# Optimization experiments

Measured on AMD Instinct MI355X. Metric: run time of the kernel, lower is better.

## Reference

```python
import jax, jax.numpy as jnp
import numpy as np

B, T, J, E = 64, 512, 64, 128
D = 2 * E  # bidaf feature dim


def _lstm_dir(x, Wih, Whh, bih, bhh, reverse):
    # x: (B, S, I); PyTorch gate order i, f, g, o
    H = Whh.shape[1]
    b = bih + bhh
    xs = jnp.swapaxes(x, 0, 1)  # (S, B, I)
    if reverse:
        xs = xs[::-1]
    pre = jnp.einsum('sbi,gi->sbg', xs, Wih) + b  # precompute input projections
    h0 = jnp.zeros((x.shape[0], H), x.dtype)

    def step(carry, pt):
        h, c = carry
        gates = pt + h @ Whh.T
        i, f, g, o = jnp.split(gates, 4, axis=-1)
        c = jax.nn.sigmoid(f) * c + jax.nn.sigmoid(i) * jnp.tanh(g)
        h = jax.nn.sigmoid(o) * jnp.tanh(c)
        return (h, c), h

    _, hs = jax.lax.scan(step, (h0, h0), pre)
    if reverse:
        hs = hs[::-1]
    return jnp.swapaxes(hs, 0, 1)  # (B, S, H)


def _bilstm(x, pf, pb):
    hf = _lstm_dir(x, pf[0], pf[1], pf[2], pf[3], False)
    hb = _lstm_dir(x, pb[0], pb[1], pb[2], pb[3], True)
    return jnp.concatenate([hf, hb], axis=-1)


def setup_inputs() -> dict:
    key = jax.random.key(0)
    ks = iter(jax.random.split(key, 40))

    def rn(shape, scale=0.05):
        return jax.random.normal(next(ks), shape, jnp.float32) * scale

    inp = {
        'c': jax.random.normal(next(ks), (B, T, D), jnp.float32),
        'q': jax.random.normal(next(ks), (B, J, D), jnp.float32),
        # trilinear attention weights (Linear(2E,1) each)
        'wc': rn((D,)), 'bc': rn((1,)),
        'wq': rn((D,)), 'bq': rn((1,)),
        'wcq': rn((D,)), 'bcq': rn((1,)),
        # modeling BiLSTM: input 8E -> hidden E, bidirectional
        'l1f_Wih': rn((4 * E, 8 * E)), 'l1f_Whh': rn((4 * E, E)), 'l1f_bih': rn((4 * E,)), 'l1f_bhh': rn((4 * E,)),
        'l1b_Wih': rn((4 * E, 8 * E)), 'l1b_Whh': rn((4 * E, E)), 'l1b_bih': rn((4 * E,)), 'l1b_bhh': rn((4 * E,)),
        # output BiLSTM: input 2E -> hidden E, bidirectional
        'l2f_Wih': rn((4 * E, 2 * E)), 'l2f_Whh': rn((4 * E, E)), 'l2f_bih': rn((4 * E,)), 'l2f_bhh': rn((4 * E,)),
        'l2b_Wih': rn((4 * E, 2 * E)), 'l2b_Whh': rn((4 * E, E)), 'l2b_bih': rn((4 * E,)), 'l2b_bhh': rn((4 * E,)),
        # span predictors Linear(10E, 1)
        'W0': rn((10 * E,)), 'b0': rn((1,)),
        'W1': rn((10 * E,)), 'b1': rn((1,)),
    }
    return inp


def reference(c, q, wc, bc, wq, bq, wcq, bcq,
              l1f_Wih, l1f_Whh, l1f_bih, l1f_bhh,
              l1b_Wih, l1b_Whh, l1b_bih, l1b_bhh,
              l2f_Wih, l2f_Whh, l2f_bih, l2f_bhh,
              l2b_Wih, l2b_Whh, l2b_bih, l2b_bhh,
              W0, b0, W1, b1):
    # fused trilinear similarity: replaces the python loop over q_len
    cq = jnp.einsum('btd,bjd,d->btj', c, q, wcq) + bcq[0]            # (B,T,J)
    s = (c @ wc + bc[0])[:, :, None] + (q @ wq + bq[0])[:, None, :] + cq
    a = jax.nn.softmax(s, axis=2)
    c2q = jnp.einsum('btj,bjd->btd', a, q)                            # context-to-query
    b_att = jax.nn.softmax(jnp.max(s, axis=2), axis=1)                # (B,T)
    q2c = jnp.einsum('bt,btd->bd', b_att, c)[:, None, :]              # (B,1,2E) broadcast over T
    g = jnp.concatenate([c, c2q, c * c2q, c * q2c * jnp.ones_like(c)], axis=-1)  # (B,T,8E)

    m = _bilstm(g, (l1f_Wih, l1f_Whh, l1f_bih, l1f_bhh), (l1b_Wih, l1b_Whh, l1b_bih, l1b_bhh))
    p1 = jax.nn.softmax(jnp.concatenate([g, m], axis=-1) @ W0 + b0[0], axis=1)
    m2 = _bilstm(m, (l2f_Wih, l2f_Whh, l2f_bih, l2f_bhh), (l2b_Wih, l2b_Whh, l2b_bih, l2b_bhh))
    p2 = jax.nn.softmax(jnp.concatenate([g, m2], axis=-1) @ W1 + b1[0], axis=1)
    return (p1, p2)
```

## Files before the change

kernel.cpp:

```cpp
#include <hip/hip_runtime.h>
#include <hip/hip_bf16.h>
#include <cstdint>
#include <cstddef>


typedef short short8v __attribute__((ext_vector_type(8)));
typedef float f32x4 __attribute__((ext_vector_type(4)));
typedef unsigned short ushort8v __attribute__((ext_vector_type(8)));
typedef unsigned short ushort4v __attribute__((ext_vector_type(4)));

static __device__ __forceinline__ float bf2f(unsigned short u) {
  return __uint_as_float(((unsigned int)u) << 16);
}
static __device__ __forceinline__ unsigned short f2bf(float f) {
  unsigned int u = __float_as_uint(f);
  return (unsigned short)((u + 0x7FFFu + ((u >> 16) & 1u)) >> 16);
}
static __device__ __forceinline__ float fsig(float x) {
  return 1.f / (1.f + __expf(-x));
}
static __device__ __forceinline__ float ftanh(float x) {
  return 1.f - 2.f / (__expf(2.f * x) + 1.f);
}

__global__ __launch_bounds__(256) void cvt_w_kernel(
    const float* __restrict__ w1f, const float* __restrict__ w1b,
    const float* __restrict__ w2f, const float* __restrict__ w2b,
    const float* __restrict__ b1fi, const float* __restrict__ b1fh,
    const float* __restrict__ b1bi, const float* __restrict__ b1bh,
    const float* __restrict__ b2fi, const float* __restrict__ b2fh,
    const float* __restrict__ b2bi, const float* __restrict__ b2bh,
    unsigned short* __restrict__ d1f, unsigned short* __restrict__ d1b,
    unsigned short* __restrict__ d2f, unsigned short* __restrict__ d2b,
    float* __restrict__ bs)
{
  const int bid = blockIdx.x, tid = threadIdx.x;
  if (bid < 1280) {
    int idx = (bid * 256 + tid) * 4;
    const float* src;
    unsigned short* dst;
    int off;
    if (idx < 524288)        { src = w1f; dst = d1f; off = idx; }
    else if (idx < 1048576)  { src = w1b; dst = d1b; off = idx - 524288; }
    else if (idx < 1179648)  { src = w2f; dst = d2f; off = idx - 1048576; }
    else                     { src = w2b; dst = d2b; off = idx - 1179648; }
    float4 f = *(const float4*)(src + off);
    ushort4v v;
    v[0] = f2bf(f.x); v[1] = f2bf(f.y); v[2] = f2bf(f.z); v[3] = f2bf(f.w);
    *(ushort4v*)(dst + off) = v;
  } else {
    int bidx = (bid - 1280) * 256 + tid;
    int which = bidx >> 9, col = bidx & 511;
    float v;
    if (which == 0)      v = b1fi[col] + b1fh[col];
    else if (which == 1) v = b1bi[col] + b1bh[col];
    else if (which == 2) v = b2fi[col] + b2fh[col];
    else                 v = b2bi[col] + b2bh[col];
    bs[bidx] = v;
  }
}

__global__ __launch_bounds__(256) void attn_kernel(
    const float* __restrict__ c, const float* __restrict__ q,
    const float* __restrict__ wc, const float* __restrict__ bc,
    const float* __restrict__ wq, const float* __restrict__ bq,
    const float* __restrict__ wcq, const float* __restrict__ bcq,
    const float* __restrict__ W0, const float* __restrict__ W1,
    __hip_bfloat16* __restrict__ g, float* __restrict__ smax,
    float* __restrict__ gz0, float* __restrict__ gz1)
{
  __shared__ unsigned short cbf[128][264];
  __shared__ unsigned short qhb[64][264];
  __shared__ unsigned short qtb[256][72];
  __shared__ unsigned short Pbuf[4][16][72];
  __shared__ float qwqs[64];
  __shared__ float qwp[4][64];
  const int b = blockIdx.x, tid = threadIdx.x;
  const int wave = tid >> 6, lane = tid & 63;
  const int t0 = blockIdx.y * 128;
  unsigned short* gbase = (unsigned short*)g;

  #pragma unroll
  for (int i = 0; i < 16; ++i) {
    int idx = tid + i * 256;
    int j = idx >> 6, d4 = (idx & 63) * 4;
    float4 v = *(const float4*)&q[((size_t)b * 64 + j) * 256 + d4];
    float4 w4 = *(const float4*)&wcq[d4];
    float4 c4 = *(const float4*)&wc[d4];
    qhb[j][d4 + 0] = f2bf(v.x * w4.x + c4.x);
    qhb[j][d4 + 1] = f2bf(v.y * w4.y + c4.y);
    qhb[j][d4 + 2] = f2bf(v.z * w4.z + c4.z);
    qhb[j][d4 + 3] = f2bf(v.w * w4.w + c4.w);
    qtb[d4 + 0][j] = f2bf(v.x);
    qtb[d4 + 1][j] = f2bf(v.y);
    qtb[d4 + 2][j] = f2bf(v.z);
    qtb[d4 + 3][j] = f2bf(v.w);
  }
  #pragma unroll
  for (int i = 0; i < 32; ++i) {
    int idx = tid + i * 256;
    int r = idx >> 6, d4 = (idx & 63) * 4;
    float4 v = *(const float4*)&c[((size_t)b * 512 + t0 + r) * 256 + d4];
    ushort4v u;
    u[0] = f2bf(v.x); u[1] = f2bf(v.y); u[2] = f2bf(v.z); u[3] = f2bf(v.w);
    *(ushort4v*)&cbf[r][d4] = u;
    *(ushort4v*)&gbase[((size_t)b * 512 + t0 + r) * 1024 + d4] = u;
  }
  __syncthreads();
  {
    float s = 0.f;
    for (int dd = 0; dd < 64; ++dd) {
      int d = wave * 64 + dd;
      s += bf2f(qtb[d][lane]) * wq[d];
    }
    qwp[wave][lane] = s;
  }
  __syncthreads();
  if (tid < 64) qwqs[tid] = qwp[0][tid] + qwp[1][tid] + qwp[2][tid] + qwp[3][tid] + bq[0];
  __syncthreads();

  const int cl = lane & 15, kg = lane >> 4;
  const float sbias = bc[0] + bcq[0];

  #pragma unroll
  for (int half = 0; half < 2; ++half) {
    const int tt = wave + half * 4;
    const int rowb = tt * 16;
    f32x4 acc[4] = {};
    #pragma unroll
    for (int kt = 0; kt < 8; ++kt) {
      short8v a = *(const short8v*)&cbf[rowb + cl][kt * 32 + kg * 8];
      #pragma unroll
      for (int jt = 0; jt < 4; ++jt) {
        short8v bq_ = *(const short8v*)&qhb[jt * 16 + cl][kt * 32 + kg * 8];
        acc[jt] = __builtin_amdgcn_mfma_f32_16x16x32_bf16(a, bq_, acc[jt], 0, 0, 0);
      }
    }
    #pragma unroll
    for (int jt = 0; jt < 4; ++jt) {
      float qadd = qwqs[jt * 16 + cl] + sbias;
      #pragma unroll
      for (int r = 0; r < 4; ++r) acc[jt][r] += qadd;
    }
    f32x4 mx = acc[0];
    #pragma unroll
    for (int jt = 1; jt < 4; ++jt)
      #pragma unroll
      for (int r = 0; r < 4; ++r) mx[r] = fmaxf(mx[r], acc[jt][r]);
    #pragma unroll
    for (int off = 1; off < 16; off <<= 1)
      #pragma unroll
      for (int r = 0; r < 4; ++r) mx[r] = fmaxf(mx[r], __shfl_xor(mx[r], off));
    f32x4 se = {0.f, 0.f, 0.f, 0.f};
    #pragma unroll
    for (int jt = 0; jt < 4; ++jt)
      #pragma unroll
      for (int r = 0; r < 4; ++r) {
        acc[jt][r] = __expf(acc[jt][r] - mx[r]);
        se[r] += acc[jt][r];
      }
    #pragma unroll
    for (int off = 1; off < 16; off <<= 1)
      #pragma unroll
      for (int r = 0; r < 4; ++r) se[r] += __shfl_xor(se[r], off);
    f32x4 inv;
    #pragma unroll
    for (int r = 0; r < 4; ++r) inv[r] = 1.f / se[r];
    #pragma unroll
    for (int jt = 0; jt < 4; ++jt)
      #pragma unroll
      for (int r = 0; r < 4; ++r)
        Pbuf[wave][4 * kg + r][jt * 16 + cl] = f2bf(acc[jt][r] * inv[r]);
    if (cl == 0) {
      #pragma unroll
      for (int r = 0; r < 4; ++r)
        smax[(size_t)b * 512 + t0 + rowb + 4 * kg + r] = mx[r];
    }
    f32x4 gz0p = {0.f, 0.f, 0.f, 0.f}, gz1p = {0.f, 0.f, 0.f, 0.f};
    for (int dt = 0; dt < 16; ++dt) {
      f32x4 ca = {0.f, 0.f, 0.f, 0.f};
      #pragma unroll
      for (int kt = 0; kt < 2; ++kt) {
        short8v pa = *(const short8v*)&Pbuf[wave][cl][kt * 32 + kg * 8];
        short8v qb_ = *(const short8v*)&qtb[dt * 16 + cl][kt * 32 + kg * 8];
        ca = __builtin_amdgcn_mfma_f32_16x16x32_bf16(pa, qb_, ca, 0, 0, 0);
      }
      int d = dt * 16 + cl;
      float w0a = W0[d], w0b_ = W0[256 + d], w0c2 = W0[512 + d];
      float w1a = W1[d], w1b2 = W1[256 + d], w1c2 = W1[512 + d];
      #pragma unroll
      for (int r = 0; r < 4; ++r) {
        int rloc = rowb + 4 * kg + r;
        float cv = bf2f(cbf[rloc][d]);
        float av = ca[r];
        float pr = cv * av;
        size_t gr = ((size_t)b * 512 + t0 + rloc) * 1024;
        gbase[gr + 256 + d] = f2bf(av);
        gbase[gr + 512 + d] = f2bf(pr);
        gz0p[r] += cv * w0a + av * w0b_ + pr * w0c2;
        gz1p[r] += cv * w1a + av * w1b2 + pr * w1c2;
      }
    }
    #pragma unroll
    for (int off = 1; off < 16; off <<= 1)
      #pragma unroll
      for (int r = 0; r < 4; ++r) {
        gz0p[r] += __shfl_xor(gz0p[r], off);
        gz1p[r] += __shfl_xor(gz1p[r], off);
      }
    if (cl == 0) {
      #pragma unroll
      for (int r = 0; r < 4; ++r) {
        size_t rw = (size_t)b * 512 + t0 + rowb + 4 * kg + r;
        gz0[rw] = gz0p[r];
        gz1[rw] = gz1p[r];
      }
    }
  }
}

__global__ __launch_bounds__(256) void batt_kernel(
    const float* __restrict__ c, const float* __restrict__ smax,
    const float* __restrict__ W0, const float* __restrict__ W1,
    __hip_bfloat16* __restrict__ g,
    float* __restrict__ gz0, float* __restrict__ gz1)
{
  __shared__ float sm[512];
  __shared__ float red[4], red2[4];
  __shared__ float q2c_s[256];
  const int b = blockIdx.x, tid = threadIdx.x;
  float v0 = smax[(size_t)b * 512 + tid];
  float v1 = smax[(size_t)b * 512 + tid + 256];
  float m = fmaxf(v0, v1);
  #pragma unroll
  for (int off = 32; off; off >>= 1) m = fmaxf(m, __shfl_xor(m, off));
  if ((tid & 63) == 0) red[tid >> 6] = m;
  __syncthreads();
  float M = fmaxf(fmaxf(red[0], red[1]), fmaxf(red[2], red[3]));
  float e0 = expf(v0 - M), e1 = expf(v1 - M);
  float ssum = e0 + e1;
  #pragma unroll
  for (int off = 32; off; off >>= 1) ssum += __shfl_xor(ssum, off);
  if ((tid & 63) == 0) red2[tid >> 6] = ssum;
  __syncthreads();
  float S = red2[0] + red2[1] + red2[2] + red2[3];
  sm[tid] = e0 / S;
  sm[tid + 256] = e1 / S;
  __syncthreads();
  float acc = 0.f;
  #pragma unroll 8
  for (int t = 0; t < 512; ++t) acc += sm[t] * c[((size_t)b * 512 + t) * 256 + tid];
  q2c_s[tid] = acc;
  __syncthreads();
  const int wave = tid >> 6, lane = tid & 63;
  float qv[4], w0c[4], w1c[4];
  #pragma unroll
  for (int r = 0; r < 4; ++r) {
    int d = lane + 64 * r;
    qv[r]  = q2c_s[d];
    w0c[r] = W0[768 + d];
    w1c[r] = W1[768 + d];
  }
  for (int t = wave; t < 512; t += 4) {
    size_t row = (size_t)b * 512 + t;
    float s0 = 0.f, s1 = 0.f;
    #pragma unroll
    for (int r = 0; r < 4; ++r) {
      int d = lane + 64 * r;
      float v = c[row * 256 + d];
      float gv = v * qv[r];
      g[row * 1024 + 768 + d] = __float2bfloat16(gv);
      s0 += gv * w0c[r];
      s1 += gv * w1c[r];
    }
    #pragma unroll
    for (int off = 32; off; off >>= 1) {
      s0 += __shfl_xor(s0, off);
      s1 += __shfl_xor(s1, off);
    }
    if (lane == 0) { gz0[row] += s0; gz1[row] += s1; }
  }
}

__global__ __launch_bounds__(256) void gemm_mfma_kernel(
    const __hip_bfloat16* __restrict__ Xg,
    const unsigned short* __restrict__ Wf, const unsigned short* __restrict__ Wb,
    const float* __restrict__ bsf, const float* __restrict__ bsb,
    __hip_bfloat16* __restrict__ Yf, __hip_bfloat16* __restrict__ Yb, int K)
{
  __shared__ unsigned short Xs[128 * 72];
  __shared__ unsigned short Ws[128 * 72];
  const unsigned short* X = (const unsigned short*)Xg;
  const unsigned short* W = blockIdx.z ? Wb : Wf;
  const float* bs = blockIdx.z ? bsb : bsf;
  __hip_bfloat16* Y = blockIdx.z ? Yb : Yf;
  const int tid = threadIdx.x;
  const int m0 = blockIdx.x * 128, n0 = blockIdx.y * 128;
  const int lane = tid & 63, wave = tid >> 6;
  const int wr = wave >> 1, wc = wave & 1;
  const int frow = lane & 15, fk = (lane >> 4) * 8;

  f32x4 acc[4][4] = {};
  for (int kt = 0; kt < K; kt += 64) {
    #pragma unroll
    for (int i = 0; i < 4; ++i) {
      int cidx = tid + 256 * i;
      int row = cidx >> 3, kc = cidx & 7;
      *(ushort8v*)&Xs[row * 72 + kc * 8] =
          *(const ushort8v*)&X[(size_t)(m0 + row) * K + kt + kc * 8];
      *(ushort8v*)&Ws[row * 72 + kc * 8] =
          *(const ushort8v*)&W[(size_t)(n0 + row) * K + kt + kc * 8];
    }
    __syncthreads();
    #pragma unroll
    for (int kk = 0; kk < 64; kk += 32) {
      short8v a[4], bfr[4];
      #pragma unroll
      for (int i = 0; i < 4; ++i)
        a[i] = *(const short8v*)&Xs[(wr * 64 + i * 16 + frow) * 72 + kk + fk];
      #pragma unroll
      for (int j = 0; j < 4; ++j)
        bfr[j] = *(const short8v*)&Ws[(wc * 64 + j * 16 + frow) * 72 + kk + fk];
      #pragma unroll
      for (int i = 0; i < 4; ++i)
        #pragma unroll
        for (int j = 0; j < 4; ++j)
          acc[i][j] = __builtin_amdgcn_mfma_f32_16x16x32_bf16(a[i], bfr[j], acc[i][j], 0, 0, 0);
    }
    __syncthreads();
  }
  const int r0 = (lane >> 4) * 4;
  #pragma unroll
  for (int j = 0; j < 4; ++j) {
    int col = n0 + wc * 64 + j * 16 + (lane & 15);
    int colp = (col & 127) * 4 + (col >> 7);
    float bsum = bs[col];
    #pragma unroll
    for (int i = 0; i < 4; ++i) {
      int rowb = m0 + wr * 64 + i * 16 + r0;
      #pragma unroll
      for (int r = 0; r < 4; ++r)
        Y[(size_t)(rowb + r) * 512 + colp] = __float2bfloat16(acc[i][j][r] + bsum);
    }
  }
}

__global__ __launch_bounds__(512, 2) void lstm_kernel(
    const __hip_bfloat16* __restrict__ pre_f, const __hip_bfloat16* __restrict__ pre_b,
    const float* __restrict__ Whh_f, const float* __restrict__ Whh_b,
    __hip_bfloat16* __restrict__ out)
{
  const int b = blockIdx.x, dir = blockIdx.y;
  const unsigned short* __restrict__ pre =
      (const unsigned short*)(dir ? pre_b : pre_f);
  const float* __restrict__ Whh = dir ? Whh_b : Whh_f;
  const int off = dir ? 128 : 0;
  const int tid = threadIdx.x;
  const int wave = tid >> 6, lane = tid & 63;
  const int cl = lane & 15;
  const int kg = lane >> 4;
  const int cell = wave * 16 + cl;

#define LOAD_BF(Q, T, DST)                                            \
  {                                                                   \
    const float* wp = Whh + (size_t)(Q * 128 + cell) * 128 + T * 32 + kg * 8; \
    float4 f0 = *(const float4*)wp;                                   \
    float4 f1 = *(const float4*)(wp + 4);                             \
    DST[0] = (short)f2bf(f0.x); DST[1] = (short)f2bf(f0.y);           \
    DST[2] = (short)f2bf(f0.z); DST[3] = (short)f2bf(f0.w);           \
    DST[4] = (short)f2bf(f1.x); DST[5] = (short)f2bf(f1.y);           \
    DST[6] = (short)f2bf(f1.z); DST[7] = (short)f2bf(f1.w);           \
    asm volatile("" : "+v"(DST));                                     \
  }
  short8v bf00, bf01, bf02, bf03, bf10, bf11, bf12, bf13;
  short8v bf20, bf21, bf22, bf23, bf30, bf31, bf32, bf33;
  LOAD_BF(0, 0, bf00) LOAD_BF(0, 1, bf01) LOAD_BF(0, 2, bf02) LOAD_BF(0, 3, bf03)
  LOAD_BF(1, 0, bf10) LOAD_BF(1, 1, bf11) LOAD_BF(1, 2, bf12) LOAD_BF(1, 3, bf13)
  LOAD_BF(2, 0, bf20) LOAD_BF(2, 1, bf21) LOAD_BF(2, 2, bf22) LOAD_BF(2, 3, bf23)
  LOAD_BF(3, 0, bf30) LOAD_BF(3, 1, bf31) LOAD_BF(3, 2, bf32) LOAD_BF(3, 3, bf33)
#undef LOAD_BF

  __shared__ unsigned short hbuf[2][128];
  if (tid < 128) { hbuf[0][tid] = 0; hbuf[1][tid] = 0; }
  __syncthreads();

  const size_t base = (size_t)b * 512;
  const int tstep = dir ? -1 : 1;
  const int t0 = dir ? 511 : 0;
  const unsigned short* prow = pre + base * 512 + cell * 4;
  unsigned short* orow = (unsigned short*)out + base * 256 + off + cell;

  int cur = 0;
  float cst = 0.f;
  f32x4 acc0 = {0.f, 0.f, 0.f, 0.f};
  f32x4 acc1 = acc0, acc2 = acc0, acc3 = acc0;

#define LSTM_STEP(P, HOUT)                                                  \
  {                                                                         \
    const unsigned short* hb = hbuf[cur];                                   \
    short8v a0 = *(const short8v*)(hb +  0 + kg * 8);                       \
    short8v a1 = *(const short8v*)(hb + 32 + kg * 8);                       \
    short8v a2 = *(const short8v*)(hb + 64 + kg * 8);                       \
    short8v a3 = *(const short8v*)(hb + 96 + kg * 8);                       \
    acc0[0] = bf2f(P[0]); acc1[0] = bf2f(P[1]);                             \
    acc2[0] = bf2f(P[2]); acc3[0] = bf2f(P[3]);                             \
    acc0 = __builtin_amdgcn_mfma_f32_16x16x32_bf16(a0, bf00, acc0, 0, 0, 0);\
    acc1 = __builtin_amdgcn_mfma_f32_16x16x32_bf16(a0, bf10, acc1, 0, 0, 0);\
    acc2 = __builtin_amdgcn_mfma_f32_16x16x32_bf16(a0, bf20, acc2, 0, 0, 0);\
    acc3 = __builtin_amdgcn_mfma_f32_16x16x32_bf16(a0, bf30, acc3, 0, 0, 0);\
    acc0 = __builtin_amdgcn_mfma_f32_16x16x32_bf16(a1, bf01, acc0, 0, 0, 0);\
    acc1 = __builtin_amdgcn_mfma_f32_16x16x32_bf16(a1, bf11, acc1, 0, 0, 0);\
    acc2 = __builtin_amdgcn_mfma_f32_16x16x32_bf16(a1, bf21, acc2, 0, 0, 0);\
    acc3 = __builtin_amdgcn_mfma_f32_16x16x32_bf16(a1, bf31, acc3, 0, 0, 0);\
    acc0 = __builtin_amdgcn_mfma_f32_16x16x32_bf16(a2, bf02, acc0, 0, 0, 0);\
    acc1 = __builtin_amdgcn_mfma_f32_16x16x32_bf16(a2, bf12, acc1, 0, 0, 0);\
    acc2 = __builtin_amdgcn_mfma_f32_16x16x32_bf16(a2, bf22, acc2, 0, 0, 0);\
    acc3 = __builtin_amdgcn_mfma_f32_16x16x32_bf16(a2, bf32, acc3, 0, 0, 0);\
    acc0 = __builtin_amdgcn_mfma_f32_16x16x32_bf16(a3, bf03, acc0, 0, 0, 0);\
    acc1 = __builtin_amdgcn_mfma_f32_16x16x32_bf16(a3, bf13, acc1, 0, 0, 0);\
    acc2 = __builtin_amdgcn_mfma_f32_16x16x32_bf16(a3, bf23, acc2, 0, 0, 0);\
    acc3 = __builtin_amdgcn_mfma_f32_16x16x32_bf16(a3, bf33, acc3, 0, 0, 0);\
    float gi_ = fsig(acc0[0]);                                              \
    float gf_ = fsig(acc1[0]);                                              \
    float gg_ = ftanh(acc2[0]);                                             \
    float go_ = fsig(acc3[0]);                                              \
    cst = gf_ * cst + gi_ * gg_;                                            \
    float hv = go_ * ftanh(cst);                                            \
    HOUT = f2bf(hv);                                                        \
    if (lane < 16) hbuf[cur ^ 1][cell] = HOUT;                              \
    __syncthreads();                                                        \
    cur ^= 1;                                                               \
  }

  for (int chunk = 0; chunk < 64; ++chunk) {
    const int tb = t0 + chunk * 8 * tstep;
    ushort4v p0 = *(const ushort4v*)(prow + (size_t)(tb)             * 512);
    ushort4v p1 = *(const ushort4v*)(prow + (size_t)(tb + 1 * tstep) * 512);
    ushort4v p2 = *(const ushort4v*)(prow + (size_t)(tb + 2 * tstep) * 512);
    ushort4v p3 = *(const ushort4v*)(prow + (size_t)(tb + 3 * tstep) * 512);
    ushort4v p4 = *(const ushort4v*)(prow + (size_t)(tb + 4 * tstep) * 512);
    ushort4v p5 = *(const ushort4v*)(prow + (size_t)(tb + 5 * tstep) * 512);
    ushort4v p6 = *(const ushort4v*)(prow + (size_t)(tb + 6 * tstep) * 512);
    ushort4v p7 = *(const ushort4v*)(prow + (size_t)(tb + 7 * tstep) * 512);
    unsigned short h0, h1, h2, h3, h4, h5, h6, h7;
    LSTM_STEP(p0, h0)
    LSTM_STEP(p1, h1)
    LSTM_STEP(p2, h2)
    LSTM_STEP(p3, h3)
    LSTM_STEP(p4, h4)
    LSTM_STEP(p5, h5)
    LSTM_STEP(p6, h6)
    LSTM_STEP(p7, h7)
    if (lane < 16) {
      orow[(size_t)(tb)             * 256] = h0;
      orow[(size_t)(tb + 1 * tstep) * 256] = h1;
      orow[(size_t)(tb + 2 * tstep) * 256] = h2;
      orow[(size_t)(tb + 3 * tstep) * 256] = h3;
      orow[(size_t)(tb + 4 * tstep) * 256] = h4;
      orow[(size_t)(tb + 5 * tstep) * 256] = h5;
      orow[(size_t)(tb + 6 * tstep) * 256] = h6;
      orow[(size_t)(tb + 7 * tstep) * 256] = h7;
    }
  }
#undef LSTM_STEP
}

__global__ __launch_bounds__(256) void logits_kernel(
    const __hip_bfloat16* __restrict__ m, const float* __restrict__ W,
    const float* __restrict__ bias, const float* __restrict__ gz,
    float* __restrict__ z)
{
  const int row = blockIdx.x * 4 + (threadIdx.x >> 6);
  const int lane = threadIdx.x & 63;
  const unsigned short* mrow = (const unsigned short*)m + (size_t)row * 256;
  float acc = 0.f;
  #pragma unroll
  for (int i = 0; i < 4; ++i) acc += bf2f(mrow[lane + 64 * i]) * W[1024 + lane + 64 * i];
  #pragma unroll
  for (int off = 32; off; off >>= 1) acc += __shfl_xor(acc, off);
  if (lane == 0) z[row] = acc + gz[row] + bias[0];
}

__global__ __launch_bounds__(512) void softmax_t_kernel(
    const float* __restrict__ z, float* __restrict__ p)
{
  const int b = blockIdx.x, t = threadIdx.x;
  __shared__ float red[8], red2[8];
  float v = z[(size_t)b * 512 + t];
  float m = v;
  #pragma unroll
  for (int off = 32; off; off >>= 1) m = fmaxf(m, __shfl_xor(m, off));
  if ((t & 63) == 0) red[t >> 6] = m;
  __syncthreads();
  float M = red[0];
  #pragma unroll
  for (int i = 1; i < 8; ++i) M = fmaxf(M, red[i]);
  float e = expf(v - M);
  float s = e;
  #pragma unroll
  for (int off = 32; off; off >>= 1) s += __shfl_xor(s, off);
  if ((t & 63) == 0) red2[t >> 6] = s;
  __syncthreads();
  float S = red2[0];
  #pragma unroll
  for (int i = 1; i < 8; ++i) S += red2[i];
  p[(size_t)b * 512 + t] = e / S;
}

extern "C" void kernel_launch(void* const* d_in, const int* in_sizes, int n_in,
                              void* d_out, int out_size, void* d_ws, size_t ws_size,
                              hipStream_t stream)
{
  const float* c   = (const float*)d_in[0];
  const float* q   = (const float*)d_in[1];
  const float* wc  = (const float*)d_in[2];
  const float* bc  = (const float*)d_in[3];
  const float* wq  = (const float*)d_in[4];
  const float* bq  = (const float*)d_in[5];
  const float* wcq = (const float*)d_in[6];
  const float* bcq = (const float*)d_in[7];
  const float* l1f_Wih = (const float*)d_in[8];
  const float* l1f_Whh = (const float*)d_in[9];
  const float* l1f_bih = (const float*)d_in[10];
  const float* l1f_bhh = (const float*)d_in[11];
  const float* l1b_Wih = (const float*)d_in[12];
  const float* l1b_Whh = (const float*)d_in[13];
  const float* l1b_bih = (const float*)d_in[14];
  const float* l1b_bhh = (const float*)d_in[15];
  const float* l2f_Wih = (const float*)d_in[16];
  const float* l2f_Whh = (const float*)d_in[17];
  const float* l2f_bih = (const float*)d_in[18];
  const float* l2f_bhh = (const float*)d_in[19];
  const float* l2b_Wih = (const float*)d_in[20];
  const float* l2b_Whh = (const float*)d_in[21];
  const float* l2b_bih = (const float*)d_in[22];
  const float* l2b_bhh = (const float*)d_in[23];
  const float* W0 = (const float*)d_in[24];
  const float* b0 = (const float*)d_in[25];
  const float* W1 = (const float*)d_in[26];
  const float* b1 = (const float*)d_in[27];

  const size_t required = 137371648u;
  if (ws_size < required) return;

  char* wsb = (char*)d_ws;
  __hip_bfloat16* gbf = (__hip_bfloat16*)wsb;
  __hip_bfloat16* m   = (__hip_bfloat16*)wsb;
  __hip_bfloat16* m2  = (__hip_bfloat16*)(wsb + 33554432);
  __hip_bfloat16* pref = (__hip_bfloat16*)(wsb + 67108864);
  __hip_bfloat16* preb = (__hip_bfloat16*)(wsb + 100663296);
  float* gz0  = (float*)(wsb + 134217728);
  float* gz1  = gz0 + 32768;
  float* smax = gz1 + 32768;
  float* z    = smax + 32768;
  unsigned short* w1f = (unsigned short*)(wsb + 134742016);
  unsigned short* w1b = (unsigned short*)(wsb + 135790592);
  unsigned short* w2f = (unsigned short*)(wsb + 136839168);
  unsigned short* w2b = (unsigned short*)(wsb + 137101312);
  float* bs = (float*)(wsb + 137363456);
  float* p1 = (float*)d_out;
  float* p2 = p1 + 32768;

  cvt_w_kernel<<<1288, 256, 0, stream>>>(l1f_Wih, l1b_Wih, l2f_Wih, l2b_Wih,
                                         l1f_bih, l1f_bhh, l1b_bih, l1b_bhh,
                                         l2f_bih, l2f_bhh, l2b_bih, l2b_bhh,
                                         w1f, w1b, w2f, w2b, bs);
  attn_kernel<<<dim3(64, 4), 256, 0, stream>>>(c, q, wc, bc, wq, bq, wcq, bcq,
                                               W0, W1, gbf, smax, gz0, gz1);
  batt_kernel<<<64, 256, 0, stream>>>(c, smax, W0, W1, gbf, gz0, gz1);

  gemm_mfma_kernel<<<dim3(256, 4, 2), 256, 0, stream>>>(
      gbf, w1f, w1b, bs, bs + 512, pref, preb, 1024);
  lstm_kernel<<<dim3(64, 2), 512, 0, stream>>>(pref, preb, l1f_Whh, l1b_Whh, m);

  logits_kernel<<<8192, 256, 0, stream>>>(m, W0, b0, gz0, z);
  softmax_t_kernel<<<64, 512, 0, stream>>>(z, p1);

  gemm_mfma_kernel<<<dim3(256, 4, 2), 256, 0, stream>>>(
      m, w2f, w2b, bs + 1024, bs + 1536, pref, preb, 256);
  lstm_kernel<<<dim3(64, 2), 512, 0, stream>>>(pref, preb, l2f_Whh, l2b_Whh, m2);

  logits_kernel<<<8192, 256, 0, stream>>>(m2, W1, b1, gz1, z);
  softmax_t_kernel<<<64, 512, 0, stream>>>(z, p2);
}
```

Measured before the change: 967.1 us.

## Split LSTM recurrence across 16 waves with gate-interleaved MFMA columns

The LSTM kernel now runs 1024 threads (16 waves) per batch/direction block instead of 512. Each wave computes 32 gate columns laid out interleaved (i,f,g,o per cell), with 8 MFMAs per step instead of 16. Activations are gathered across lanes with shuffles to form the cell update. This halves the serial MFMA chain per step and the weight registers per thread, at the cost of a wider barrier across more waves, extra shuffles, and scalar 2-byte pre-activation loads in place of vector loads.

```diff
diff --git a/kernel.cpp b/kernel.cpp
--- a/kernel.cpp
+++ b/kernel.cpp
@@ -345,7 +345,7 @@
   }
 }
 
-__global__ __launch_bounds__(512, 2) void lstm_kernel(
+__global__ __launch_bounds__(1024) void lstm_kernel(
     const __hip_bfloat16* __restrict__ pre_f, const __hip_bfloat16* __restrict__ pre_b,
     const float* __restrict__ Whh_f, const float* __restrict__ Whh_b,
     __hip_bfloat16* __restrict__ out)
@@ -359,25 +359,28 @@
   const int wave = tid >> 6, lane = tid & 63;
   const int cl = lane & 15;
   const int kg = lane >> 4;
-  const int cell = wave * 16 + cl;
-
-#define LOAD_BF(Q, T, DST)                                            \
-  {                                                                   \
-    const float* wp = Whh + (size_t)(Q * 128 + cell) * 128 + T * 32 + kg * 8; \
-    float4 f0 = *(const float4*)wp;                                   \
-    float4 f1 = *(const float4*)(wp + 4);                             \
-    DST[0] = (short)f2bf(f0.x); DST[1] = (short)f2bf(f0.y);           \
-    DST[2] = (short)f2bf(f0.z); DST[3] = (short)f2bf(f0.w);           \
-    DST[4] = (short)f2bf(f1.x); DST[5] = (short)f2bf(f1.y);           \
-    DST[6] = (short)f2bf(f1.z); DST[7] = (short)f2bf(f1.w);           \
-    asm volatile("" : "+v"(DST));                                     \
-  }
-  short8v bf00, bf01, bf02, bf03, bf10, bf11, bf12, bf13;
-  short8v bf20, bf21, bf22, bf23, bf30, bf31, bf32, bf33;
-  LOAD_BF(0, 0, bf00) LOAD_BF(0, 1, bf01) LOAD_BF(0, 2, bf02) LOAD_BF(0, 3, bf03)
-  LOAD_BF(1, 0, bf10) LOAD_BF(1, 1, bf11) LOAD_BF(1, 2, bf12) LOAD_BF(1, 3, bf13)
-  LOAD_BF(2, 0, bf20) LOAD_BF(2, 1, bf21) LOAD_BF(2, 2, bf22) LOAD_BF(2, 3, bf23)
-  LOAD_BF(3, 0, bf30) LOAD_BF(3, 1, bf31) LOAD_BF(3, 2, bf32) LOAD_BF(3, 3, bf33)
+  const int q3 = cl & 3;
+  const int lbase = lane & ~3;
+  const int cellA = 8 * wave + (cl >> 2);
+  const int cellB = cellA + 4;
+  const int nA = 32 * wave + cl;
+  const int nB = nA + 16;
+
+#define LOAD_BF(N, KT, DST)                                                 \
+  {                                                                         \
+    const float* wp = Whh + (size_t)(((N) & 3) * 128 + ((N) >> 2)) * 128 +  \
+                      (KT) * 32 + kg * 8;                                   \
+    float4 f0 = *(const float4*)wp;                                         \
+    float4 f1 = *(const float4*)(wp + 4);                                   \
+    DST[0] = (short)f2bf(f0.x); DST[1] = (short)f2bf(f0.y);                 \
+    DST[2] = (short)f2bf(f0.z); DST[3] = (short)f2bf(f0.w);                 \
+    DST[4] = (short)f2bf(f1.x); DST[5] = (short)f2bf(f1.y);                 \
+    DST[6] = (short)f2bf(f1.z); DST[7] = (short)f2bf(f1.w);                 \
+    asm volatile("" : "+v"(DST));                                           \
+  }
+  short8v b00, b01, b02, b03, b10, b11, b12, b13;
+  LOAD_BF(nA, 0, b00) LOAD_BF(nA, 1, b01) LOAD_BF(nA, 2, b02) LOAD_BF(nA, 3, b03)
+  LOAD_BF(nB, 0, b10) LOAD_BF(nB, 1, b11) LOAD_BF(nB, 2, b12) LOAD_BF(nB, 3, b13)
 #undef LOAD_BF
 
   __shared__ unsigned short hbuf[2][128];
@@ -387,79 +390,98 @@
   const size_t base = (size_t)b * 512;
   const int tstep = dir ? -1 : 1;
   const int t0 = dir ? 511 : 0;
-  const unsigned short* prow = pre + base * 512 + cell * 4;
-  unsigned short* orow = (unsigned short*)out + base * 256 + off + cell;
+  const unsigned short* prowA = pre + base * 512 + nA;
+  const unsigned short* prowB = pre + base * 512 + nB;
+  unsigned short* orowA = (unsigned short*)out + base * 256 + off + cellA;
+  unsigned short* orowB = (unsigned short*)out + base * 256 + off + cellB;
+  const bool writer = (kg == 0) && (q3 == 0);
 
   int cur = 0;
-  float cst = 0.f;
+  float cstA = 0.f, cstB = 0.f;
   f32x4 acc0 = {0.f, 0.f, 0.f, 0.f};
-  f32x4 acc1 = acc0, acc2 = acc0, acc3 = acc0;
-
-#define LSTM_STEP(P, HOUT)                                                  \
+  f32x4 acc1 = acc0;
+
+#define LSTM_STEP(PA, PB, HA, HB)                                           \
   {                                                                         \
     const unsigned short* hb = hbuf[cur];                                   \
     short8v a0 = *(const short8v*)(hb +  0 + kg * 8);                       \
     short8v a1 = *(const short8v*)(hb + 32 + kg * 8);                       \
     short8v a2 = *(const short8v*)(hb + 64 + kg * 8);                       \
     short8v a3 = *(const short8v*)(hb + 96 + kg * 8);                       \
-    acc0[0] = bf2f(P[0]); acc1[0] = bf2f(P[1]);                             \
-    acc2[0] = bf2f(P[2]); acc3[0] = bf2f(P[3]);                             \
-    acc0 = __builtin_amdgcn_mfma_f32_16x16x32_bf16(a0, bf00, acc0, 0, 0, 0);\
-    acc1 = __builtin_amdgcn_mfma_f32_16x16x32_bf16(a0, bf10, acc1, 0, 0, 0);\
-    acc2 = __builtin_amdgcn_mfma_f32_16x16x32_bf16(a0, bf20, acc2, 0, 0, 0);\
-    acc3 = __builtin_amdgcn_mfma_f32_16x16x32_bf16(a0, bf30, acc3, 0, 0, 0);\
-    acc0 = __builtin_amdgcn_mfma_f32_16x16x32_bf16(a1, bf01, acc0, 0, 0, 0);\
-    acc1 = __builtin_amdgcn_mfma_f32_16x16x32_bf16(a1, bf11, acc1, 0, 0, 0);\
-    acc2 = __builtin_amdgcn_mfma_f32_16x16x32_bf16(a1, bf21, acc2, 0, 0, 0);\
-    acc3 = __builtin_amdgcn_mfma_f32_16x16x32_bf16(a1, bf31, acc3, 0, 0, 0);\
-    acc0 = __builtin_amdgcn_mfma_f32_16x16x32_bf16(a2, bf02, acc0, 0, 0, 0);\
-    acc1 = __builtin_amdgcn_mfma_f32_16x16x32_bf16(a2, bf12, acc1, 0, 0, 0);\
-    acc2 = __builtin_amdgcn_mfma_f32_16x16x32_bf16(a2, bf22, acc2, 0, 0, 0);\
-    acc3 = __builtin_amdgcn_mfma_f32_16x16x32_bf16(a2, bf32, acc3, 0, 0, 0);\
-    acc0 = __builtin_amdgcn_mfma_f32_16x16x32_bf16(a3, bf03, acc0, 0, 0, 0);\
-    acc1 = __builtin_amdgcn_mfma_f32_16x16x32_bf16(a3, bf13, acc1, 0, 0, 0);\
-    acc2 = __builtin_amdgcn_mfma_f32_16x16x32_bf16(a3, bf23, acc2, 0, 0, 0);\
-    acc3 = __builtin_amdgcn_mfma_f32_16x16x32_bf16(a3, bf33, acc3, 0, 0, 0);\
-    float gi_ = fsig(acc0[0]);                                              \
-    float gf_ = fsig(acc1[0]);                                              \
-    float gg_ = ftanh(acc2[0]);                                             \
-    float go_ = fsig(acc3[0]);                                              \
-    cst = gf_ * cst + gi_ * gg_;                                            \
-    float hv = go_ * ftanh(cst);                                            \
-    HOUT = f2bf(hv);                                                        \
-    if (lane < 16) hbuf[cur ^ 1][cell] = HOUT;                              \
+    acc0[0] = bf2f(PA); acc1[0] = bf2f(PB);                                 \
+    acc0 = __builtin_amdgcn_mfma_f32_16x16x32_bf16(a0, b00, acc0, 0, 0, 0); \
+    acc1 = __builtin_amdgcn_mfma_f32_16x16x32_bf16(a0, b10, acc1, 0, 0, 0); \
+    acc0 = __builtin_amdgcn_mfma_f32_16x16x32_bf16(a1, b01, acc0, 0, 0, 0); \
+    acc1 = __builtin_amdgcn_mfma_f32_16x16x32_bf16(a1, b11, acc1, 0, 0, 0); \
+    acc0 = __builtin_amdgcn_mfma_f32_16x16x32_bf16(a2, b02, acc0, 0, 0, 0); \
+    acc1 = __builtin_amdgcn_mfma_f32_16x16x32_bf16(a2, b12, acc1, 0, 0, 0); \
+    acc0 = __builtin_amdgcn_mfma_f32_16x16x32_bf16(a3, b03, acc0, 0, 0, 0); \
+    acc1 = __builtin_amdgcn_mfma_f32_16x16x32_bf16(a3, b13, acc1, 0, 0, 0); \
+    float x0 = acc0[0], x1 = acc1[0];                                       \
+    float av0 = (q3 == 2) ? ftanh(x0) : fsig(x0);                           \
+    float av1 = (q3 == 2) ? ftanh(x1) : fsig(x1);                           \
+    float gi0 = __shfl(av0, lbase),     gf0 = __shfl(av0, lbase + 1);       \
+    float gg0 = __shfl(av0, lbase + 2), go0 = __shfl(av0, lbase + 3);       \
+    float gi1 = __shfl(av1, lbase),     gf1 = __shfl(av1, lbase + 1);       \
+    float gg1 = __shfl(av1, lbase + 2), go1 = __shfl(av1, lbase + 3);       \
+    cstA = gf0 * cstA + gi0 * gg0;                                          \
+    cstB = gf1 * cstB + gi1 * gg1;                                          \
+    float hv0 = go0 * ftanh(cstA);                                          \
+    float hv1 = go1 * ftanh(cstB);                                          \
+    HA = f2bf(hv0); HB = f2bf(hv1);                                         \
+    if (writer) {                                                           \
+      hbuf[cur ^ 1][cellA] = HA;                                            \
+      hbuf[cur ^ 1][cellB] = HB;                                            \
+    }                                                                       \
     __syncthreads();                                                        \
     cur ^= 1;                                                               \
   }
 
   for (int chunk = 0; chunk < 64; ++chunk) {
     const int tb = t0 + chunk * 8 * tstep;
-    ushort4v p0 = *(const ushort4v*)(prow + (size_t)(tb)             * 512);
-    ushort4v p1 = *(const ushort4v*)(prow + (size_t)(tb + 1 * tstep) * 512);
-    ushort4v p2 = *(const ushort4v*)(prow + (size_t)(tb + 2 * tstep) * 512);
-    ushort4v p3 = *(const ushort4v*)(prow + (size_t)(tb + 3 * tstep) * 512);
-    ushort4v p4 = *(const ushort4v*)(prow + (size_t)(tb + 4 * tstep) * 512);
-    ushort4v p5 = *(const ushort4v*)(prow + (size_t)(tb + 5 * tstep) * 512);
-    ushort4v p6 = *(const ushort4v*)(prow + (size_t)(tb + 6 * tstep) * 512);
-    ushort4v p7 = *(const ushort4v*)(prow + (size_t)(tb + 7 * tstep) * 512);
-    unsigned short h0, h1, h2, h3, h4, h5, h6, h7;
-    LSTM_STEP(p0, h0)
-    LSTM_STEP(p1, h1)
-    LSTM_STEP(p2, h2)
-    LSTM_STEP(p3, h3)
-    LSTM_STEP(p4, h4)
-    LSTM_STEP(p5, h5)
-    LSTM_STEP(p6, h6)
-    LSTM_STEP(p7, h7)
-    if (lane < 16) {
-      orow[(size_t)(tb)             * 256] = h0;
-      orow[(size_t)(tb + 1 * tstep) * 256] = h1;
-      orow[(size_t)(tb + 2 * tstep) * 256] = h2;
-      orow[(size_t)(tb + 3 * tstep) * 256] = h3;
-      orow[(size_t)(tb + 4 * tstep) * 256] = h4;
-      orow[(size_t)(tb + 5 * tstep) * 256] = h5;
-      orow[(size_t)(tb + 6 * tstep) * 256] = h6;
-      orow[(size_t)(tb + 7 * tstep) * 256] = h7;
+    unsigned short pa0 = prowA[(size_t)(tb)             * 512];
+    unsigned short pb0 = prowB[(size_t)(tb)             * 512];
+    unsigned short pa1 = prowA[(size_t)(tb + 1 * tstep) * 512];
+    unsigned short pb1 = prowB[(size_t)(tb + 1 * tstep) * 512];
+    unsigned short pa2 = prowA[(size_t)(tb + 2 * tstep) * 512];
+    unsigned short pb2 = prowB[(size_t)(tb + 2 * tstep) * 512];
+    unsigned short pa3 = prowA[(size_t)(tb + 3 * tstep) * 512];
+    unsigned short pb3 = prowB[(size_t)(tb + 3 * tstep) * 512];
+    unsigned short pa4 = prowA[(size_t)(tb + 4 * tstep) * 512];
+    unsigned short pb4 = prowB[(size_t)(tb + 4 * tstep) * 512];
+    unsigned short pa5 = prowA[(size_t)(tb + 5 * tstep) * 512];
+    unsigned short pb5 = prowB[(size_t)(tb + 5 * tstep) * 512];
+    unsigned short pa6 = prowA[(size_t)(tb + 6 * tstep) * 512];
+    unsigned short pb6 = prowB[(size_t)(tb + 6 * tstep) * 512];
+    unsigned short pa7 = prowA[(size_t)(tb + 7 * tstep) * 512];
+    unsigned short pb7 = prowB[(size_t)(tb + 7 * tstep) * 512];
+    unsigned short hA0, hA1, hA2, hA3, hA4, hA5, hA6, hA7;
+    unsigned short hB0, hB1, hB2, hB3, hB4, hB5, hB6, hB7;
+    LSTM_STEP(pa0, pb0, hA0, hB0)
+    LSTM_STEP(pa1, pb1, hA1, hB1)
+    LSTM_STEP(pa2, pb2, hA2, hB2)
+    LSTM_STEP(pa3, pb3, hA3, hB3)
+    LSTM_STEP(pa4, pb4, hA4, hB4)
+    LSTM_STEP(pa5, pb5, hA5, hB5)
+    LSTM_STEP(pa6, pb6, hA6, hB6)
+    LSTM_STEP(pa7, pb7, hA7, hB7)
+    if (writer) {
+      orowA[(size_t)(tb)             * 256] = hA0;
+      orowA[(size_t)(tb + 1 * tstep) * 256] = hA1;
+      orowA[(size_t)(tb + 2 * tstep) * 256] = hA2;
+      orowA[(size_t)(tb + 3 * tstep) * 256] = hA3;
+      orowA[(size_t)(tb + 4 * tstep) * 256] = hA4;
+      orowA[(size_t)(tb + 5 * tstep) * 256] = hA5;
+      orowA[(size_t)(tb + 6 * tstep) * 256] = hA6;
+      orowA[(size_t)(tb + 7 * tstep) * 256] = hA7;
+      orowB[(size_t)(tb)             * 256] = hB0;
+      orowB[(size_t)(tb + 1 * tstep) * 256] = hB1;
+      orowB[(size_t)(tb + 2 * tstep) * 256] = hB2;
+      orowB[(size_t)(tb + 3 * tstep) * 256] = hB3;
+      orowB[(size_t)(tb + 4 * tstep) * 256] = hB4;
+      orowB[(size_t)(tb + 5 * tstep) * 256] = hB5;
+      orowB[(size_t)(tb + 6 * tstep) * 256] = hB6;
+      orowB[(size_t)(tb + 7 * tstep) * 256] = hB7;
     }
   }
 #undef LSTM_STEP
@@ -571,14 +593,14 @@
 
   gemm_mfma_kernel<<<dim3(256, 4, 2), 256, 0, stream>>>(
       gbf, w1f, w1b, bs, bs + 512, pref, preb, 1024);
-  lstm_kernel<<<dim3(64, 2), 512, 0, stream>>>(pref, preb, l1f_Whh, l1b_Whh, m);
+  lstm_kernel<<<dim3(64, 2), 1024, 0, stream>>>(pref, preb, l1f_Whh, l1b_Whh, m);
 
   logits_kernel<<<8192, 256, 0, stream>>>(m, W0, b0, gz0, z);
   softmax_t_kernel<<<64, 512, 0, stream>>>(z, p1);
 
   gemm_mfma_kernel<<<dim3(256, 4, 2), 256, 0, stream>>>(
       m, w2f, w2b, bs + 1024, bs + 1536, pref, preb, 256);
-  lstm_kernel<<<dim3(64, 2), 512, 0, stream>>>(pref, preb, l2f_Whh, l2b_Whh, m2);
+  lstm_kernel<<<dim3(64, 2), 1024, 0, stream>>>(pref, preb, l2f_Whh, l2b_Whh, m2);
 
   logits_kernel<<<8192, 256, 0, stream>>>(m2, W1, b1, gz1, z);
   softmax_t_kernel<<<64, 512, 0, stream>>>(z, p2);
```

Result: slower. 1.556 ms (+60.8%).

## Pre-swizzle g and layer-1 weights; use direct global-to-LDS loads in GEMM1

Applied to the files above, without the earlier changes.

Producers of the g feature matrix and the bf16 conversion of layer-1 input weights now write data in an XOR-swizzled column order within each 64-element chunk. A new GEMM kernel for the first projection loads tiles straight into LDS with global_load_lds and reads the MFMA fragments through the matching swizzle. This removes the register staging and LDS padding of the old tile loads and avoids bank conflicts. The cost is that the layout is coupled across the attention, batt, conversion and GEMM kernels, and the kernel still uses a single LDS buffer with no double buffering.

```diff
diff --git a/kernel.cpp b/kernel.cpp
--- a/kernel.cpp
+++ b/kernel.cpp
@@ -21,6 +21,16 @@
 }
 static __device__ __forceinline__ float ftanh(float x) {
   return 1.f - 2.f / (__expf(2.f * x) + 1.f);
+}
+static __device__ __forceinline__ int swzcol(int row, int col) {
+  int ch = col >> 3;
+  int cs = (ch & ~7) | ((ch ^ row) & 7);
+  return cs * 8 + (col & 7);
+}
+static __device__ __forceinline__ void gld_lds16(const void* g, void* l) {
+  __builtin_amdgcn_global_load_lds(
+      (const __attribute__((address_space(1))) unsigned int*)g,
+      (__attribute__((address_space(3))) unsigned int*)l, 16, 0, 0);
 }
 
 __global__ __launch_bounds__(256) void cvt_w_kernel(
@@ -40,14 +50,20 @@
     const float* src;
     unsigned short* dst;
     int off;
-    if (idx < 524288)        { src = w1f; dst = d1f; off = idx; }
-    else if (idx < 1048576)  { src = w1b; dst = d1b; off = idx - 524288; }
-    else if (idx < 1179648)  { src = w2f; dst = d2f; off = idx - 1048576; }
-    else                     { src = w2b; dst = d2b; off = idx - 1179648; }
+    bool swz;
+    if (idx < 524288)        { src = w1f; dst = d1f; off = idx; swz = true; }
+    else if (idx < 1048576)  { src = w1b; dst = d1b; off = idx - 524288; swz = true; }
+    else if (idx < 1179648)  { src = w2f; dst = d2f; off = idx - 1048576; swz = false; }
+    else                     { src = w2b; dst = d2b; off = idx - 1179648; swz = false; }
     float4 f = *(const float4*)(src + off);
     ushort4v v;
     v[0] = f2bf(f.x); v[1] = f2bf(f.y); v[2] = f2bf(f.z); v[3] = f2bf(f.w);
-    *(ushort4v*)(dst + off) = v;
+    if (swz) {
+      int row = off >> 10, col = off & 1023;
+      *(ushort4v*)(dst + ((size_t)row << 10) + swzcol(row, col)) = v;
+    } else {
+      *(ushort4v*)(dst + off) = v;
+    }
   } else {
     int bidx = (bid - 1280) * 256 + tid;
     int which = bidx >> 9, col = bidx & 511;
@@ -104,7 +120,7 @@
     ushort4v u;
     u[0] = f2bf(v.x); u[1] = f2bf(v.y); u[2] = f2bf(v.z); u[3] = f2bf(v.w);
     *(ushort4v*)&cbf[r][d4] = u;
-    *(ushort4v*)&gbase[((size_t)b * 512 + t0 + r) * 1024 + d4] = u;
+    *(ushort4v*)&gbase[((size_t)b * 512 + t0 + r) * 1024 + swzcol(r, d4)] = u;
   }
   __syncthreads();
   {
@@ -195,8 +211,8 @@
         float av = ca[r];
         float pr = cv * av;
         size_t gr = ((size_t)b * 512 + t0 + rloc) * 1024;
-        gbase[gr + 256 + d] = f2bf(av);
-        gbase[gr + 512 + d] = f2bf(pr);
+        gbase[gr + swzcol(rloc, 256 + d)] = f2bf(av);
+        gbase[gr + swzcol(rloc, 512 + d)] = f2bf(pr);
         gz0p[r] += cv * w0a + av * w0b_ + pr * w0c2;
         gz1p[r] += cv * w1a + av * w1b2 + pr * w1c2;
       }
@@ -269,7 +285,7 @@
       int d = lane + 64 * r;
       float v = c[row * 256 + d];
       float gv = v * qv[r];
-      g[row * 1024 + 768 + d] = __float2bfloat16(gv);
+      g[row * 1024 + swzcol(t, 768 + d)] = __float2bfloat16(gv);
       s0 += gv * w0c[r];
       s1 += gv * w1c[r];
     }
@@ -279,6 +295,70 @@
       s1 += __shfl_xor(s1, off);
     }
     if (lane == 0) { gz0[row] += s0; gz1[row] += s1; }
+  }
+}
+
+__global__ __launch_bounds__(256) void gemm1_kernel(
+    const unsigned short* __restrict__ X,
+    const unsigned short* __restrict__ Wf, const unsigned short* __restrict__ Wb,
+    const float* __restrict__ bsf, const float* __restrict__ bsb,
+    __hip_bfloat16* __restrict__ Yf, __hip_bfloat16* __restrict__ Yb)
+{
+  __shared__ unsigned short Xs[128 * 64];
+  __shared__ unsigned short Ws[128 * 64];
+  const unsigned short* W = blockIdx.z ? Wb : Wf;
+  const float* bs = blockIdx.z ? bsb : bsf;
+  __hip_bfloat16* Y = blockIdx.z ? Yb : Yf;
+  const int tid = threadIdx.x;
+  const int m0 = blockIdx.x * 128, n0 = blockIdx.y * 128;
+  const int lane = tid & 63, wave = tid >> 6;
+  const int wr = wave >> 1, wc = wave & 1;
+  const int frow = lane & 15, kg = lane >> 4;
+  const int r7 = frow & 7;
+  const int cid_l = wave * 64 + lane;
+
+  f32x4 acc[4][4] = {};
+  for (int kt = 0; kt < 1024; kt += 64) {
+    #pragma unroll
+    for (int i = 0; i < 4; ++i) {
+      int cb = i * 256 + wave * 64;
+      int cid = i * 256 + cid_l;
+      int row = cid >> 3, ch = cid & 7;
+      gld_lds16(X + (size_t)(m0 + row) * 1024 + kt + ch * 8, Xs + cb * 8);
+      gld_lds16(W + (size_t)(n0 + row) * 1024 + kt + ch * 8, Ws + cb * 8);
+    }
+    __syncthreads();
+    #pragma unroll
+    for (int kk = 0; kk < 64; kk += 32) {
+      const int pc = (((kk >> 3) + kg) ^ r7) * 8;
+      short8v a[4], bfr[4];
+      #pragma unroll
+      for (int i = 0; i < 4; ++i)
+        a[i] = *(const short8v*)&Xs[(wr * 64 + i * 16 + frow) * 64 + pc];
+      #pragma unroll
+      for (int j = 0; j < 4; ++j)
+        bfr[j] = *(const short8v*)&Ws[(wc * 64 + j * 16 + frow) * 64 + pc];
+      #pragma unroll
+      for (int i = 0; i < 4; ++i)
+        #pragma unroll
+        for (int j = 0; j < 4; ++j)
+          acc[i][j] = __builtin_amdgcn_mfma_f32_16x16x32_bf16(a[i], bfr[j], acc[i][j], 0, 0, 0);
+    }
+    __syncthreads();
+  }
+  const int r0 = kg * 4;
+  #pragma unroll
+  for (int j = 0; j < 4; ++j) {
+    int col = n0 + wc * 64 + j * 16 + frow;
+    int colp = (col & 127) * 4 + (col >> 7);
+    float bsum = bs[col];
+    #pragma unroll
+    for (int i = 0; i < 4; ++i) {
+      int rowb = m0 + wr * 64 + i * 16 + r0;
+      #pragma unroll
+      for (int r = 0; r < 4; ++r)
+        Y[(size_t)(rowb + r) * 512 + colp] = __float2bfloat16(acc[i][j][r] + bsum);
+    }
   }
 }
 
@@ -569,8 +649,8 @@
                                                W0, W1, gbf, smax, gz0, gz1);
   batt_kernel<<<64, 256, 0, stream>>>(c, smax, W0, W1, gbf, gz0, gz1);
 
-  gemm_mfma_kernel<<<dim3(256, 4, 2), 256, 0, stream>>>(
-      gbf, w1f, w1b, bs, bs + 512, pref, preb, 1024);
+  gemm1_kernel<<<dim3(256, 4, 2), 256, 0, stream>>>(
+      (const unsigned short*)gbf, w1f, w1b, bs, bs + 512, pref, preb);
   lstm_kernel<<<dim3(64, 2), 512, 0, stream>>>(pref, preb, l1f_Whh, l1b_Whh, m);
 
   logits_kernel<<<8192, 256, 0, stream>>>(m, W0, b0, gz0, z);
```

Result: no change. 963.0 us (-0.4%).
